# Kernel optimization log

Measured on AMD Instinct MI355X. Metric: run time of the kernel, lower is better.

## Reference

```python
import jax, jax.numpy as jnp
import numpy as np
import math

B, N, D, H = 1, 128, 256, 8
DK = D // H

def setup_inputs() -> dict:
    key = jax.random.key(0)
    ks = jax.random.split(key, 8)
    query = jax.random.normal(ks[0], (B, N, N, D), dtype=jnp.float32)
    key_t = jax.random.normal(ks[1], (B, N, N, D), dtype=jnp.float32)
    value = jax.random.normal(ks[2], (B, N, N, D), dtype=jnp.float32)
    mask = jax.random.randint(ks[3], (B, N, N, N), 0, 2).astype(jnp.bool_)
    s = 1.0 / math.sqrt(D)
    # torch nn.Linear weights: [out_features, in_features]
    Wk = jax.random.uniform(ks[4], (D, D), dtype=jnp.float32, minval=-s, maxval=s)
    Wv = jax.random.uniform(ks[5], (D, D), dtype=jnp.float32, minval=-s, maxval=s)
    Wq = jax.random.uniform(ks[6], (D, D), dtype=jnp.float32, minval=-s, maxval=s)
    Wo = jax.random.uniform(ks[7], (D, D), dtype=jnp.float32, minval=-s, maxval=s)
    return {"query": query, "key": key_t, "value": value, "mask": mask,
            "Wq": Wq, "Wk": Wk, "Wv": Wv, "Wo": Wo}

def reference(query, key, value, mask, Wq, Wk, Wv, Wo):
    b, n = query.shape[0], query.shape[1]
    # linear projections (no bias), then split heads -> [b, n, n, h, d_k]
    q = (query @ Wq.T).reshape(b, n, n, H, DK)
    k = (key @ Wk.T).reshape(b, n, n, H, DK)
    v = (value @ Wv.T).reshape(b, n, n, H, DK)
    scale = 1.0 / math.sqrt(DK)
    neg = jnp.float32(-1e9)
    m = mask[..., None]  # [b, n, n, n, 1] broadcast over heads
    # row attention: edge (x,y) attends over edges (x,z)
    scores_r = jnp.einsum('bxyhd,bxzhd->bxyzh', q, k) * scale
    scores_r = jnp.where(m, neg, scores_r)
    # column attention: edge (x,y) attends over edges (z,y)
    scores_l = jnp.einsum('bxyhd,bzyhd->bxyzh', q, k) * scale
    scores_l = jnp.where(m, neg, scores_l)
    scores = jnp.concatenate((scores_r, scores_l), axis=3)  # [b,n,n,2n,h]
    att = jax.nn.softmax(scores, axis=3)
    att_r, att_l = att[:, :, :, :n], att[:, :, :, n:]
    x_r = jnp.einsum('bxyzh,bxzhd->bxyhd', att_r, v)
    x_l = jnp.einsum('bxyzh,bzyhd->bxyhd', att_l, v)
    x = (x_r + x_l).reshape(b, n, n, D)
    return x @ Wo.T
```

## Files before the change

kernel.cpp:

```cpp
#include <hip/hip_runtime.h>
#include <hip/hip_bf16.h>
#include <math.h>

#define N_DIM 128
#define NH 8
#define DKH 32
#define M_ROWS (N_DIM * N_DIM)

typedef __attribute__((ext_vector_type(8))) short bf16x8;
typedef __attribute__((ext_vector_type(4))) float f32x4;

__device__ inline ushort f2b(float x) {
    union { __hip_bfloat16 b; ushort u; } c;
    c.b = __float2bfloat16(x);
    return c.u;
}

#define GLDS(src, dst) \
    __builtin_amdgcn_global_load_lds((const __attribute__((address_space(1))) void*)(src), \
                                     (__attribute__((address_space(3))) void*)(dst), 16, 0, 0)

__global__ __launch_bounds__(256) void prep_kernel(const int* __restrict__ mask,
                                                   ulonglong2* __restrict__ P,
                                                   ulonglong2* __restrict__ PT,
                                                   const float* __restrict__ w0,
                                                   const float* __restrict__ w1,
                                                   const float* __restrict__ w2,
                                                   const float* __restrict__ w3,
                                                   ushort* __restrict__ wout) {
    if (blockIdx.x < 4096) {
        const int row = blockIdx.x * 4 + (threadIdx.x >> 6);
        const int lane = threadIdx.x & 63;
        const int* mrow = mask + (size_t)row * 128;
        unsigned long long lo = __ballot(mrow[lane] != 0);
        unsigned long long hi = __ballot(mrow[64 + lane] != 0);
        if (lane == 0) {
            ulonglong2 v; v.x = lo; v.y = hi;
            P[row] = v;
            PT[(row & 127) * 128 + (row >> 7)] = v;
        }
    } else {
        const int b = blockIdx.x - 4096;
        const int m = b >> 6;
        const float* src = (m == 0) ? w0 : (m == 1) ? w1 : (m == 2) ? w2 : w3;
        const int off = (b & 63) * 1024 + threadIdx.x * 4;
        float4 v = *(const float4*)(src + off);
        union { ushort u[4]; short4 s4; } p;
        p.u[0] = f2b(v.x); p.u[1] = f2b(v.y); p.u[2] = f2b(v.z); p.u[3] = f2b(v.w);
        *(short4*)(wout + (size_t)m * 65536 + off) = p.s4;
    }
}

template <bool AF32, bool OBF16, bool BATCHED>
__global__ __launch_bounds__(512) void gemm2(const void* __restrict__ A0,
                                             const void* __restrict__ A1,
                                             const void* __restrict__ A2,
                                             const ushort* __restrict__ Wbase,
                                             void* __restrict__ Cbase,
                                             float oscale0) {
    __shared__ ushort As[2][32 * 64];
    __shared__ ushort Ws[2][256 * 64];
    const int tid = threadIdx.x;
    const int w = tid >> 6, l = tid & 63;
    const int lr = l & 15, g = l >> 4;
    const int row0 = blockIdx.x * 32;

    const void* Ain = A0;
    const ushort* W = Wbase;
    float oscale = oscale0;
    size_t coff = 0;
    if (BATCHED) {
        const int y = blockIdx.y;
        Ain = (y == 0) ? A0 : (y == 1) ? A1 : A2;
        W += (size_t)y * 65536;
        coff = (size_t)y * (M_ROWS * 256);
        oscale = (y == 0) ? oscale0 : 1.0f;
    }

    const int lrow = l >> 3;
    const int kof = ((l & 7) ^ lrow) * 8;

    auto stage = [&](int t, int buf) {
        const int kbase = t * 64;
#pragma unroll
        for (int i = 0; i < 4; i++) {
            const int chunk = i * 8 + w;
            GLDS(W + (size_t)(chunk * 8 + lrow) * 256 + kbase + kof,
                 &Ws[buf][chunk * 512]);
        }
        if (AF32) {
            const float* Af = (const float*)Ain;
            const int r = tid >> 4, k0 = (tid & 15) * 4;
            float4 v = *(const float4*)(Af + (size_t)(row0 + r) * 256 + kbase + k0);
            union { ushort u[4]; short4 s4; } p;
            p.u[0] = f2b(v.x); p.u[1] = f2b(v.y); p.u[2] = f2b(v.z); p.u[3] = f2b(v.w);
            int byte = (r * 128 + k0 * 2) ^ ((r & 7) << 4);
            *(short4*)((char*)&As[buf][0] + byte) = p.s4;
        } else {
            if (w < 4) {
                const ushort* Ab = (const ushort*)Ain;
                GLDS(Ab + (size_t)(row0 + w * 8 + lrow) * 256 + kbase + kof,
                     &As[buf][w * 512]);
            }
        }
    };

    f32x4 acc[2][2];
    const f32x4 zero = {0.f, 0.f, 0.f, 0.f};
    acc[0][0] = zero; acc[0][1] = zero; acc[1][0] = zero; acc[1][1] = zero;

    stage(0, 0);
    __syncthreads();

#pragma unroll
    for (int t = 0; t < 4; t++) {
        const int cur = t & 1;
        if (t < 3) stage(t + 1, cur ^ 1);
#pragma unroll
        for (int kk = 0; kk < 2; kk++) {
            bf16x8 a[2], b[2];
#pragma unroll
            for (int fr = 0; fr < 2; fr++) {
                const int r = fr * 16 + lr;
                int byte = r * 128 + kk * 64 + g * 16;
                byte ^= (r & 7) << 4;
                a[fr] = *(const bf16x8*)((const char*)&As[cur][0] + byte);
            }
#pragma unroll
            for (int fc = 0; fc < 2; fc++) {
                const int r = w * 32 + fc * 16 + lr;
                int byte = r * 128 + kk * 64 + g * 16;
                byte ^= (r & 7) << 4;
                b[fc] = *(const bf16x8*)((const char*)&Ws[cur][0] + byte);
            }
#pragma unroll
            for (int fr = 0; fr < 2; fr++)
#pragma unroll
                for (int fc = 0; fc < 2; fc++)
                    acc[fr][fc] = __builtin_amdgcn_mfma_f32_16x16x32_bf16(a[fr], b[fc], acc[fr][fc], 0, 0, 0);
        }
        __syncthreads();
    }

#pragma unroll
    for (int fr = 0; fr < 2; fr++)
#pragma unroll
        for (int fc = 0; fc < 2; fc++)
#pragma unroll
            for (int j = 0; j < 4; j++) {
                const int row = row0 + fr * 16 + g * 4 + j;
                const int col = w * 32 + fc * 16 + lr;
                const float vv = acc[fr][fc][j] * oscale;
                if (OBF16) ((ushort*)Cbase)[coff + (size_t)row * 256 + col] = f2b(vv);
                else       ((float*)Cbase)[(size_t)row * 256 + col] = vv;
            }
}

template <int PASS>
__global__ __launch_bounds__(256) void attn_pass(const ushort* __restrict__ qb,
                                                 const ushort* __restrict__ kb,
                                                 const ushort* __restrict__ vb,
                                                 const ulonglong2* __restrict__ Pm,
                                                 float* __restrict__ ml,
                                                 float* __restrict__ sl,
                                                 float* __restrict__ Pl,
                                                 ushort* __restrict__ xb) {
    __shared__ ushort Ks[128 * 40];
    __shared__ ushort Vt[32 * 128];
    __shared__ ushort Ats[128 * 128];
    __shared__ ulonglong2 Ms[128];
    __shared__ float mlq[128], slq[128];

    const int tid = threadIdx.x;
    const int fixed = blockIdx.x >> 3;
    const int h = blockIdx.x & 7;

    int base, stride;
    if (PASS == 0) {
        base = (fixed * NH + h) * DKH;
        stride = N_DIM * NH * DKH;
    } else {
        base = fixed * N_DIM * NH * DKH + h * DKH;
        stride = NH * DKH;
    }

    const int w = tid >> 6;
    const int lane = tid & 63;
    const int lr = lane & 15;
    const int g = lane >> 4;
    const int rbase = w * 32;

    if (tid < 128) {
        Ms[tid] = Pm[fixed * 128 + tid];
        if (PASS == 1) mlq[tid] = ml[(fixed * NH + h) * N_DIM + tid];
    } else if (PASS == 1) {
        slq[tid - 128] = sl[(fixed * NH + h) * N_DIM + (tid - 128)];
    }

    float plv[2][2][4];
    if (PASS == 1) {
#pragma unroll
        for (int fr = 0; fr < 2; fr++)
#pragma unroll
            for (int j = 0; j < 4; j++) {
                const int row = rbase + fr * 16 + g * 4 + j;
#pragma unroll
                for (int fc = 0; fc < 2; fc++) {
                    const int d = fc * 16 + lr;
                    plv[fr][fc][j] = Pl[((size_t)(fixed * NH + h) * N_DIM + row) * DKH + d];
                }
            }
    }

    bf16x8 aq[2];
#pragma unroll
    for (int fr = 0; fr < 2; fr++)
        aq[fr] = *(const bf16x8*)(qb + (size_t)base +
                                  (size_t)(rbase + fr * 16 + lr) * stride + g * 8);

#pragma unroll
    for (int i = 0; i < 2; i++) {
        int idx = tid + i * 256;
        int r = idx >> 2, d0 = (idx & 3) * 8;
        size_t goff = (size_t)base + (size_t)r * stride + d0;
        int4 kv = *(const int4*)(kb + goff);
        *(int4*)&Ks[r * 40 + d0] = kv;
        union { int4 v4; ushort u[8]; } uu;
        uu.v4 = *(const int4*)(vb + goff);
#pragma unroll
        for (int j = 0; j < 8; j++) {
            int d = d0 + j;
            int byte = d * 256 + r * 2;
            byte ^= (d & 7) << 4;
            Vt[byte >> 1] = uu.u[j];
        }
    }
    __syncthreads();

    f32x4 s[2][8];
    const f32x4 zero = {0.f, 0.f, 0.f, 0.f};
#pragma unroll
    for (int fc = 0; fc < 8; fc++) {
        bf16x8 bk = *(const bf16x8*)&Ks[(fc * 16 + lr) * 40 + g * 8];
#pragma unroll
        for (int fr = 0; fr < 2; fr++)
            s[fr][fc] = __builtin_amdgcn_mfma_f32_16x16x32_bf16(aq[fr], bk, zero, 0, 0, 0);
    }

    float mx[2][4], sm[2][4];
#pragma unroll
    for (int fr = 0; fr < 2; fr++) {
#pragma unroll
        for (int j = 0; j < 4; j++) {
            const int row = rbase + fr * 16 + g * 4 + j;
            const ulonglong2 mb = Ms[row];
            const unsigned long long mls = mb.x >> lr;
            const unsigned long long mhs = mb.y >> lr;
            float mmax = -3.0e38f;
#pragma unroll
            for (int fc = 0; fc < 8; fc++) {
                const int bit = (int)(((fc < 4 ? mls : mhs) >> ((fc & 3) * 16)) & 1ull);
                float val = bit ? -1.0e9f : s[fr][fc][j];
                s[fr][fc][j] = val;
                mmax = fmaxf(mmax, val);
            }
            mmax = fmaxf(mmax, __shfl_xor(mmax, 1));
            mmax = fmaxf(mmax, __shfl_xor(mmax, 2));
            mmax = fmaxf(mmax, __shfl_xor(mmax, 4));
            mmax = fmaxf(mmax, __shfl_xor(mmax, 8));
            float ssum = 0.f;
#pragma unroll
            for (int fc = 0; fc < 8; fc++) {
                const int col = fc * 16 + lr;
                float e = __expf(s[fr][fc][j] - mmax);
                ssum += e;
                int byte = row * 256 + col * 2;
                byte ^= (row & 7) << 4;
                Ats[byte >> 1] = f2b(e);
            }
            ssum += __shfl_xor(ssum, 1);
            ssum += __shfl_xor(ssum, 2);
            ssum += __shfl_xor(ssum, 4);
            ssum += __shfl_xor(ssum, 8);
            mx[fr][j] = mmax;
            sm[fr][j] = ssum;
        }
    }
    __syncthreads();

    f32x4 p[2][2];
    p[0][0] = zero; p[0][1] = zero; p[1][0] = zero; p[1][1] = zero;
#pragma unroll
    for (int ks = 0; ks < 4; ks++) {
        bf16x8 pa[2];
#pragma unroll
        for (int fr = 0; fr < 2; fr++) {
            const int row = rbase + fr * 16 + lr;
            int byte = row * 256 + ks * 64 + g * 16;
            byte ^= (row & 7) << 4;
            pa[fr] = *(const bf16x8*)&Ats[byte >> 1];
        }
#pragma unroll
        for (int fc = 0; fc < 2; fc++) {
            const int rd = fc * 16 + lr;
            int byte = rd * 256 + ks * 64 + g * 16;
            byte ^= (rd & 7) << 4;
            bf16x8 vbf = *(const bf16x8*)&Vt[byte >> 1];
#pragma unroll
            for (int fr = 0; fr < 2; fr++)
                p[fr][fc] = __builtin_amdgcn_mfma_f32_16x16x32_bf16(pa[fr], vbf, p[fr][fc], 0, 0, 0);
        }
    }

    if (PASS == 0) {
#pragma unroll
        for (int fr = 0; fr < 2; fr++) {
#pragma unroll
            for (int j = 0; j < 4; j++) {
                const int row = rbase + fr * 16 + g * 4 + j;
                if (lr == 0) {
                    ml[((size_t)row * NH + h) * N_DIM + fixed] = mx[fr][j];
                    sl[((size_t)row * NH + h) * N_DIM + fixed] = sm[fr][j];
                }
#pragma unroll
                for (int fc = 0; fc < 2; fc++) {
                    const int d = fc * 16 + lr;
                    Pl[((size_t)(row * NH + h) * N_DIM + fixed) * DKH + d] = p[fr][fc][j];
                }
            }
        }
    } else {
#pragma unroll
        for (int fr = 0; fr < 2; fr++) {
#pragma unroll
            for (int j = 0; j < 4; j++) {
                const int row = rbase + fr * 16 + g * 4 + j;
                const float mr = mx[fr][j], sr = sm[fr][j];
                const float mlv = mlq[row], slv = slq[row];
                const float m = fmaxf(mr, mlv);
                const float cr = __expf(mr - m), cl = __expf(mlv - m);
                const float inv = 1.0f / (sr * cr + slv * cl);
#pragma unroll
                for (int fc = 0; fc < 2; fc++) {
                    const int d = fc * 16 + lr;
                    const float o = (p[fr][fc][j] * cr + plv[fr][fc][j] * cl) * inv;
                    xb[((size_t)fixed * N_DIM + row) * 256 + h * DKH + d] = f2b(o);
                }
            }
        }
    }
}

extern "C" void kernel_launch(void* const* d_in, const int* in_sizes, int n_in,
                              void* d_out, int out_size, void* d_ws, size_t ws_size,
                              hipStream_t stream) {
    const float* query = (const float*)d_in[0];
    const float* key_t = (const float*)d_in[1];
    const float* value = (const float*)d_in[2];
    const int*   mask  = (const int*)d_in[3];
    const float* Wq    = (const float*)d_in[4];
    const float* Wk    = (const float*)d_in[5];
    const float* Wv    = (const float*)d_in[6];
    const float* Wo    = (const float*)d_in[7];

    const size_t MB = 1024 * 1024;
    char* ws = (char*)d_ws;
    ushort*     qb = (ushort*)ws;
    ushort*     kb = qb + (size_t)M_ROWS * 256;
    ushort*     vb = kb + (size_t)M_ROWS * 256;
    ushort*     xb = (ushort*)(ws + 24 * MB);
    float*      Pl = (float*)(ws + 32 * MB);
    float*      ml = (float*)(ws + 48 * MB);
    float*      sl = (float*)(ws + 48 * MB + 512 * 1024);
    ushort*     Wb = (ushort*)(ws + 49 * MB);
    ulonglong2* Pp = (ulonglong2*)(ws + 50 * MB);
    ulonglong2* PT = (ulonglong2*)(ws + 50 * MB + 256 * 1024);

    const float qscale = 0.17677669529663687f;

    prep_kernel<<<4352, 256, 0, stream>>>(mask, Pp, PT, Wq, Wk, Wv, Wo, Wb);
    gemm2<true, true, true><<<dim3(M_ROWS / 32, 3), 512, 0, stream>>>(
        query, key_t, value, Wb, qb, qscale);
    attn_pass<0><<<N_DIM * NH, 256, 0, stream>>>(qb, kb, vb, PT, ml, sl, Pl, xb);
    attn_pass<1><<<N_DIM * NH, 256, 0, stream>>>(qb, kb, vb, Pp, ml, sl, Pl, xb);
    gemm2<false, false, false><<<dim3(M_ROWS / 32, 1), 512, 0, stream>>>(
        xb, nullptr, nullptr, Wb + 3 * 65536, d_out, 1.0f);
}
```

Before: 167.0 us.

## Restructure projection GEMM to preload weight half in LDS and stream A from registers

The GEMM now splits the 256 output columns across two blocks of 256 threads. Each block loads its full 128x256 bf16 weight slice into LDS once with a single sync, and reads A fragments straight from global memory into registers, converting to bf16 where needed, instead of double-buffering A and W tiles through LDS. This drops the per-k-step barriers and LDS staging for A. In exchange each A row is read twice (once per column block), global load latency is exposed inside the MFMA loop, and 64KB of LDS per block may limit occupancy. Separately, the attention pass 1 now loads ml/sl straight into registers instead of staging them in shared memory.

```diff
diff --git a/kernel.cpp b/kernel.cpp
--- a/kernel.cpp
+++ b/kernel.cpp
@@ -52,94 +52,79 @@
 }
 
 template <bool AF32, bool OBF16, bool BATCHED>
-__global__ __launch_bounds__(512) void gemm2(const void* __restrict__ A0,
+__global__ __launch_bounds__(256) void gemm3(const void* __restrict__ A0,
                                              const void* __restrict__ A1,
                                              const void* __restrict__ A2,
                                              const ushort* __restrict__ Wbase,
                                              void* __restrict__ Cbase,
                                              float oscale0) {
-    __shared__ ushort As[2][32 * 64];
-    __shared__ ushort Ws[2][256 * 64];
+    __shared__ ushort Ws[128 * 256];
     const int tid = threadIdx.x;
     const int w = tid >> 6, l = tid & 63;
     const int lr = l & 15, g = l >> 4;
     const int row0 = blockIdx.x * 32;
+    const int col0 = blockIdx.y * 128;
 
     const void* Ain = A0;
     const ushort* W = Wbase;
     float oscale = oscale0;
     size_t coff = 0;
     if (BATCHED) {
-        const int y = blockIdx.y;
-        Ain = (y == 0) ? A0 : (y == 1) ? A1 : A2;
-        W += (size_t)y * 65536;
-        coff = (size_t)y * (M_ROWS * 256);
-        oscale = (y == 0) ? oscale0 : 1.0f;
-    }
-
-    const int lrow = l >> 3;
-    const int kof = ((l & 7) ^ lrow) * 8;
-
-    auto stage = [&](int t, int buf) {
-        const int kbase = t * 64;
-#pragma unroll
-        for (int i = 0; i < 4; i++) {
-            const int chunk = i * 8 + w;
-            GLDS(W + (size_t)(chunk * 8 + lrow) * 256 + kbase + kof,
-                 &Ws[buf][chunk * 512]);
-        }
-        if (AF32) {
-            const float* Af = (const float*)Ain;
-            const int r = tid >> 4, k0 = (tid & 15) * 4;
-            float4 v = *(const float4*)(Af + (size_t)(row0 + r) * 256 + kbase + k0);
-            union { ushort u[4]; short4 s4; } p;
-            p.u[0] = f2b(v.x); p.u[1] = f2b(v.y); p.u[2] = f2b(v.z); p.u[3] = f2b(v.w);
-            int byte = (r * 128 + k0 * 2) ^ ((r & 7) << 4);
-            *(short4*)((char*)&As[buf][0] + byte) = p.s4;
-        } else {
-            if (w < 4) {
-                const ushort* Ab = (const ushort*)Ain;
-                GLDS(Ab + (size_t)(row0 + w * 8 + lrow) * 256 + kbase + kof,
-                     &As[buf][w * 512]);
-            }
-        }
-    };
+        const int z = blockIdx.z;
+        Ain = (z == 0) ? A0 : (z == 1) ? A1 : A2;
+        W += (size_t)z * 65536;
+        coff = (size_t)z * ((size_t)M_ROWS * 256);
+        oscale = (z == 0) ? oscale0 : 1.0f;
+    }
+
+    {
+        const int lsub = l >> 5;
+        const int lc31 = l & 31;
+#pragma unroll
+        for (int i = 0; i < 16; i++) {
+            const int c2 = w * 16 + i;
+            const int r = c2 * 2 + lsub;
+            GLDS(W + (size_t)(col0 + r) * 256 + ((lc31 ^ (r & 7)) * 8),
+                 &Ws[c2 * 512]);
+        }
+    }
+    __syncthreads();
+
+    const float* Af = (const float*)Ain;
+    const ushort* Ab = (const ushort*)Ain;
 
     f32x4 acc[2][2];
     const f32x4 zero = {0.f, 0.f, 0.f, 0.f};
     acc[0][0] = zero; acc[0][1] = zero; acc[1][0] = zero; acc[1][1] = zero;
 
-    stage(0, 0);
-    __syncthreads();
-
-#pragma unroll
-    for (int t = 0; t < 4; t++) {
-        const int cur = t & 1;
-        if (t < 3) stage(t + 1, cur ^ 1);
-#pragma unroll
-        for (int kk = 0; kk < 2; kk++) {
-            bf16x8 a[2], b[2];
-#pragma unroll
-            for (int fr = 0; fr < 2; fr++) {
-                const int r = fr * 16 + lr;
-                int byte = r * 128 + kk * 64 + g * 16;
-                byte ^= (r & 7) << 4;
-                a[fr] = *(const bf16x8*)((const char*)&As[cur][0] + byte);
-            }
-#pragma unroll
-            for (int fc = 0; fc < 2; fc++) {
-                const int r = w * 32 + fc * 16 + lr;
-                int byte = r * 128 + kk * 64 + g * 16;
-                byte ^= (r & 7) << 4;
-                b[fc] = *(const bf16x8*)((const char*)&Ws[cur][0] + byte);
-            }
+#pragma unroll
+    for (int ks = 0; ks < 8; ks++) {
+        bf16x8 a[2];
+#pragma unroll
+        for (int fr = 0; fr < 2; fr++) {
+            const size_t off = (size_t)(row0 + fr * 16 + lr) * 256 + ks * 32 + g * 8;
+            if (AF32) {
+                float4 v0 = *(const float4*)(Af + off);
+                float4 v1 = *(const float4*)(Af + off + 4);
+                union { ushort u[8]; bf16x8 b; } pk;
+                pk.u[0] = f2b(v0.x); pk.u[1] = f2b(v0.y);
+                pk.u[2] = f2b(v0.z); pk.u[3] = f2b(v0.w);
+                pk.u[4] = f2b(v1.x); pk.u[5] = f2b(v1.y);
+                pk.u[6] = f2b(v1.z); pk.u[7] = f2b(v1.w);
+                a[fr] = pk.b;
+            } else {
+                a[fr] = *(const bf16x8*)(Ab + off);
+            }
+        }
+#pragma unroll
+        for (int fc = 0; fc < 2; fc++) {
+            const int rw = w * 32 + fc * 16 + lr;
+            bf16x8 b = *(const bf16x8*)((const char*)Ws + rw * 512 +
+                                        (((ks * 4 + g) ^ (rw & 7)) * 16));
 #pragma unroll
             for (int fr = 0; fr < 2; fr++)
-#pragma unroll
-                for (int fc = 0; fc < 2; fc++)
-                    acc[fr][fc] = __builtin_amdgcn_mfma_f32_16x16x32_bf16(a[fr], b[fc], acc[fr][fc], 0, 0, 0);
-        }
-        __syncthreads();
+                acc[fr][fc] = __builtin_amdgcn_mfma_f32_16x16x32_bf16(a[fr], b, acc[fr][fc], 0, 0, 0);
+        }
     }
 
 #pragma unroll
@@ -149,7 +134,7 @@
 #pragma unroll
             for (int j = 0; j < 4; j++) {
                 const int row = row0 + fr * 16 + g * 4 + j;
-                const int col = w * 32 + fc * 16 + lr;
+                const int col = col0 + w * 32 + fc * 16 + lr;
                 const float vv = acc[fr][fc][j] * oscale;
                 if (OBF16) ((ushort*)Cbase)[coff + (size_t)row * 256 + col] = f2b(vv);
                 else       ((float*)Cbase)[(size_t)row * 256 + col] = vv;
@@ -169,7 +154,6 @@
     __shared__ ushort Vt[32 * 128];
     __shared__ ushort Ats[128 * 128];
     __shared__ ulonglong2 Ms[128];
-    __shared__ float mlq[128], slq[128];
 
     const int tid = threadIdx.x;
     const int fixed = blockIdx.x >> 3;
@@ -190,20 +174,17 @@
     const int g = lane >> 4;
     const int rbase = w * 32;
 
-    if (tid < 128) {
-        Ms[tid] = Pm[fixed * 128 + tid];
-        if (PASS == 1) mlq[tid] = ml[(fixed * NH + h) * N_DIM + tid];
-    } else if (PASS == 1) {
-        slq[tid - 128] = sl[(fixed * NH + h) * N_DIM + (tid - 128)];
-    }
-
-    float plv[2][2][4];
+    if (tid < 128) Ms[tid] = Pm[fixed * 128 + tid];
+
+    float plv[2][2][4], mlv_r[2][4], slv_r[2][4];
     if (PASS == 1) {
 #pragma unroll
         for (int fr = 0; fr < 2; fr++)
 #pragma unroll
             for (int j = 0; j < 4; j++) {
                 const int row = rbase + fr * 16 + g * 4 + j;
+                mlv_r[fr][j] = ml[(size_t)(fixed * NH + h) * N_DIM + row];
+                slv_r[fr][j] = sl[(size_t)(fixed * NH + h) * N_DIM + row];
 #pragma unroll
                 for (int fc = 0; fc < 2; fc++) {
                     const int d = fc * 16 + lr;
@@ -336,7 +317,7 @@
             for (int j = 0; j < 4; j++) {
                 const int row = rbase + fr * 16 + g * 4 + j;
                 const float mr = mx[fr][j], sr = sm[fr][j];
-                const float mlv = mlq[row], slv = slq[row];
+                const float mlv = mlv_r[fr][j], slv = slv_r[fr][j];
                 const float m = fmaxf(mr, mlv);
                 const float cr = __expf(mr - m), cl = __expf(mlv - m);
                 const float inv = 1.0f / (sr * cr + slv * cl);
@@ -379,10 +360,10 @@
     const float qscale = 0.17677669529663687f;
 
     prep_kernel<<<4352, 256, 0, stream>>>(mask, Pp, PT, Wq, Wk, Wv, Wo, Wb);
-    gemm2<true, true, true><<<dim3(M_ROWS / 32, 3), 512, 0, stream>>>(
+    gemm3<true, true, true><<<dim3(M_ROWS / 32, 2, 3), 256, 0, stream>>>(
         query, key_t, value, Wb, qb, qscale);
     attn_pass<0><<<N_DIM * NH, 256, 0, stream>>>(qb, kb, vb, PT, ml, sl, Pl, xb);
     attn_pass<1><<<N_DIM * NH, 256, 0, stream>>>(qb, kb, vb, Pp, ml, sl, Pl, xb);
-    gemm2<false, false, false><<<dim3(M_ROWS / 32, 1), 512, 0, stream>>>(
+    gemm3<false, false, false><<<dim3(M_ROWS / 32, 2, 1), 256, 0, stream>>>(
         xb, nullptr, nullptr, Wb + 3 * 65536, d_out, 1.0f);
 }
```

Result: slower. 198.9 us (+19.1%).
